# Optimization experiments

Hardware: AMD Instinct MI355X
Metric: run time of the kernel (lower is better)

The kernel has to match this reference:

```python
import jax, jax.numpy as jnp
import numpy as np

B, L, H, D, N, R, K = 1, 2048, 2048, 4096, 16, 128, 4


def setup_inputs() -> dict:
    key = jax.random.key(0)
    ks = jax.random.split(key, 10)
    s = 0.02
    x = jax.random.normal(ks[0], (B, L, H), dtype=jnp.float32)
    W_in = jax.random.normal(ks[1], (H, 2 * D), dtype=jnp.float32) * s
    conv_w = jax.random.normal(ks[2], (K, D), dtype=jnp.float32) * s  # depthwise causal conv
    conv_b = jnp.zeros((D,), dtype=jnp.float32)
    W_x = jax.random.normal(ks[3], (D, R + 2 * N), dtype=jnp.float32) * s
    W_dt = jax.random.normal(ks[4], (R, D), dtype=jnp.float32) * (R ** -0.5)
    # dt bias initialized so softplus(b_dt) ~ dt in [1e-3, 1e-1]
    dt = jnp.exp(jax.random.uniform(ks[5], (D,)) * (np.log(0.1) - np.log(1e-3)) + np.log(1e-3))
    b_dt = dt + jnp.log(-jnp.expm1(-dt))
    A_log = jnp.broadcast_to(jnp.log(jnp.arange(1, N + 1, dtype=jnp.float32)), (D, N))
    D_param = jnp.ones((D,), dtype=jnp.float32)
    W_out = jax.random.normal(ks[6], (D, H), dtype=jnp.float32) * s
    return {"x": x, "W_in": W_in, "conv_w": conv_w, "conv_b": conv_b,
            "W_x": W_x, "W_dt": W_dt, "b_dt": b_dt, "A_log": A_log,
            "D_param": D_param, "W_out": W_out}


def _mamba_fwd(x, W_in, conv_w, conv_b, W_x, W_dt, b_dt, A_log, D_param, W_out):
    silu = jax.nn.silu
    # in_proj then chunk into hidden / gate: [B,L,D] each
    proj = x @ W_in
    hs, gate = jnp.split(proj, 2, axis=-1)
    # causal depthwise conv along sequence (pad K-1 on the left)
    hs_pad = jnp.pad(hs, ((0, 0), (K - 1, 0), (0, 0)))
    conv = sum(hs_pad[:, k:k + L, :] * conv_w[k] for k in range(K)) + conv_b
    hs = silu(conv)  # [B,L,D]
    # ssm parameters
    ssm_p = hs @ W_x  # [B,L,R+2N]
    dt_in, Bm, Cm = jnp.split(ssm_p, [R, R + N], axis=-1)
    dt = jax.nn.softplus(dt_in @ W_dt + b_dt)  # [B,L,D]
    A = -jnp.exp(A_log)  # [D,N]
    dA = jnp.exp(dt[..., None] * A)                       # [B,L,D,N]
    dBu = dt[..., None] * Bm[:, :, None, :] * hs[..., None]  # [B,L,D,N]

    def step(s, inp):
        dA_t, dBu_t, C_t = inp
        s = dA_t * s + dBu_t                 # [B,D,N]
        y = jnp.einsum('bdn,bn->bd', s, C_t)
        return s, y

    s0 = jnp.zeros((B, D, N), dtype=x.dtype)
    xs = (jnp.moveaxis(dA, 1, 0), jnp.moveaxis(dBu, 1, 0), jnp.moveaxis(Cm, 1, 0))
    _, ys = jax.lax.scan(step, s0, xs)       # [L,B,D]
    y = jnp.moveaxis(ys, 0, 1)               # [B,L,D]
    y = y + hs * D_param
    y = y * silu(gate)
    return y @ W_out                          # [B,L,H]


def reference(x, W_in, conv_w, conv_b, W_x, W_dt, b_dt, A_log, D_param, W_out):
    return _mamba_fwd(x, W_in, conv_w, conv_b, W_x, W_dt, b_dt, A_log, D_param, W_out)
```

## Files before the change

### kernel.cpp

```cpp
#include <hip/hip_runtime.h>
#include <hip/hip_bf16.h>

typedef short short8 __attribute__((ext_vector_type(8)));
typedef float floatx4 __attribute__((ext_vector_type(4)));
using bf16 = __hip_bfloat16;

static constexpr int L = 2048, H = 2048, D = 4096, NS = 16, R = 128, KC = 4;
static constexpr int CCH = 64, TCH = L / CCH;
static constexpr int KSP = 16, KCHUNK = 4096 / KSP;
static constexpr int ZOUT = 4, KOUT = 4096 / ZOUT;

__device__ __forceinline__ void g2lds16(const void* g, void* l) {
  __builtin_amdgcn_global_load_lds((const __attribute__((address_space(1))) unsigned int*)g,
                                   (__attribute__((address_space(3))) unsigned int*)l,
                                   16, 0, 0);
}

__global__ void cast_f2b(const float* __restrict__ in, bf16* __restrict__ out, int n) {
  int i = blockIdx.x * 256 + threadIdx.x;
  if (i < n) out[i] = __float2bfloat16(in[i]);
}

__global__ void transpose_cast(const float* __restrict__ in, bf16* __restrict__ out,
                               int Rr, int Cc) {
  __shared__ float tile[32][33];
  int c0 = blockIdx.x * 32, r0 = blockIdx.y * 32;
  int tx = threadIdx.x, ty = threadIdx.y;
#pragma unroll
  for (int i = 0; i < 32; i += 8)
    tile[ty + i][tx] = in[(size_t)(r0 + ty + i) * Cc + (c0 + tx)];
  __syncthreads();
#pragma unroll
  for (int i = 0; i < 32; i += 8)
    out[(size_t)(c0 + ty + i) * Rr + (r0 + tx)] = __float2bfloat16(tile[tx][ty + i]);
}

template <int MODE>
__global__ __launch_bounds__(256) void gemm_async(
    const bf16* __restrict__ A, int lda,
    const bf16* __restrict__ Bt, int ldb,
    bf16* __restrict__ Cb, bf16* __restrict__ Cb2, int ldc, int K) {
  __shared__ short As[2 * 128 * 32];
  __shared__ short Bs[2 * 128 * 32];
  const int m0 = blockIdx.y * 128, n0 = blockIdx.x * 128;
  const int kbeg = (MODE == 3) ? blockIdx.z * K : 0;
  const int tid = threadIdx.x;
  const int lane = tid & 63;
  const int wave = tid >> 6;
  const int wm = (wave >> 1) * 64, wn = (wave & 1) * 64;
  const int lr = lane & 15, kq = lane >> 4;
  const int sr = lane >> 2, sc = (lane & 3) * 8;

  const bf16* Ab = A + (size_t)(m0 + wave * 16 + sr) * lda + sc;
  const bf16* Bb = Bt + (size_t)(n0 + wave * 16 + sr) * ldb + sc;
  short* Asw = &As[wave * 16 * 32];
  short* Bsw = &Bs[wave * 16 * 32];

  floatx4 acc[4][4];
#pragma unroll
  for (int i = 0; i < 4; i++)
#pragma unroll
    for (int j = 0; j < 4; j++)
#pragma unroll
      for (int r = 0; r < 4; r++) acc[i][j][r] = 0.f;

  for (int k0 = kbeg; k0 < kbeg + K; k0 += 64) {
    __syncthreads();
#pragma unroll
    for (int h = 0; h < 2; h++) {
      int kk = k0 + h * 32;
#pragma unroll
      for (int j = 0; j < 2; j++) {
        g2lds16(Ab + (size_t)j * 64 * lda + kk, Asw + h * 4096 + j * 64 * 32);
        g2lds16(Bb + (size_t)j * 64 * ldb + kk, Bsw + h * 4096 + j * 64 * 32);
      }
    }
    __syncthreads();
#pragma unroll
    for (int h = 0; h < 2; h++) {
      short8 af[4], bfr[4];
#pragma unroll
      for (int i = 0; i < 4; i++)
        af[i] = *(const short8*)(&As[h * 4096 + (wm + i * 16 + lr) * 32 + kq * 8]);
#pragma unroll
      for (int j = 0; j < 4; j++)
        bfr[j] = *(const short8*)(&Bs[h * 4096 + (wn + j * 16 + lr) * 32 + kq * 8]);
#pragma unroll
      for (int i = 0; i < 4; i++)
#pragma unroll
        for (int j = 0; j < 4; j++)
          acc[i][j] = __builtin_amdgcn_mfma_f32_16x16x32_bf16(af[i], bfr[j], acc[i][j], 0, 0, 0);
    }
  }

  bf16* base = Cb;
  int coff = 0, ld = ldc;
  if (MODE == 2) {
    if (n0 >= D) { base = Cb2; coff = D; }
    ld = D;
  }
  if (MODE == 3) base = Cb + (size_t)blockIdx.z * L * ldc;
  const int rb = kq * 4;
#pragma unroll
  for (int i = 0; i < 4; i++)
#pragma unroll
    for (int j = 0; j < 4; j++) {
      int col = n0 + wn + j * 16 + lr - coff;
      int row = m0 + wm + i * 16 + rb;
#pragma unroll
      for (int r = 0; r < 4; r++)
        base[(size_t)(row + r) * ld + col] = __float2bfloat16(acc[i][j][r]);
    }
}

__global__ void out_reduce(const unsigned short* __restrict__ P, float* __restrict__ out) {
  int i = blockIdx.x * 256 + threadIdx.x;
  const size_t LH = (size_t)L * H;
  float acc[8];
#pragma unroll
  for (int e = 0; e < 8; e++) acc[e] = 0.f;
#pragma unroll
  for (int z = 0; z < ZOUT; z++) {
    short8 v = *(const short8*)(P + z * LH + (size_t)i * 8);
#pragma unroll
    for (int e = 0; e < 8; e++)
      acc[e] += __uint_as_float(((unsigned)(unsigned short)v[e]) << 16);
  }
#pragma unroll
  for (int q = 0; q < 2; q++) {
    floatx4 o;
#pragma unroll
    for (int r = 0; r < 4; r++) o[r] = acc[q * 4 + r];
    *(floatx4*)(out + (size_t)i * 8 + q * 4) = o;
  }
}

__global__ __launch_bounds__(256) void gemm_splitk(
    const bf16* __restrict__ A, int lda,
    const bf16* __restrict__ Bt, int ldb,
    float* __restrict__ P, int ldc, int N) {
  __shared__ short As[128 * 40];
  __shared__ short Bs[128 * 40];
  const int m0 = blockIdx.y * 128, n0 = blockIdx.x * 128;
  const int kbeg = blockIdx.z * KCHUNK;
  float* C = P + (size_t)blockIdx.z * L * ldc;
  const int tid = threadIdx.x;
  const int lane = tid & 63;
  const int wave = tid >> 6;
  const int wm = (wave >> 1) * 64, wn = (wave & 1) * 64;
  const int lr = lane & 15, kq = lane >> 4;
  const int srow = tid >> 2, scol = (tid & 3) * 8;

  floatx4 acc[4][4];
#pragma unroll
  for (int i = 0; i < 4; i++)
#pragma unroll
    for (int j = 0; j < 4; j++)
#pragma unroll
      for (int r = 0; r < 4; r++) acc[i][j][r] = 0.f;

  for (int k0 = kbeg; k0 < kbeg + KCHUNK; k0 += 32) {
    __syncthreads();
#pragma unroll
    for (int h = 0; h < 2; h++) {
      int r = srow + h * 64;
      short8 va = *(const short8*)((const short*)A + (size_t)(m0 + r) * lda + k0 + scol);
      *(short8*)(&As[r * 40 + scol]) = va;
    }
#pragma unroll
    for (int h = 0; h < 2; h++) {
      int r = srow + h * 64;
      short8 vb;
      if ((n0 + r) < N) {
        vb = *(const short8*)((const short*)Bt + (size_t)(n0 + r) * ldb + k0 + scol);
      } else {
#pragma unroll
        for (int q = 0; q < 8; q++) vb[q] = 0;
      }
      *(short8*)(&Bs[r * 40 + scol]) = vb;
    }
    __syncthreads();
    short8 af[4], bfr[4];
#pragma unroll
    for (int i = 0; i < 4; i++)
      af[i] = *(const short8*)(&As[(wm + i * 16 + lr) * 40 + kq * 8]);
#pragma unroll
    for (int j = 0; j < 4; j++)
      bfr[j] = *(const short8*)(&Bs[(wn + j * 16 + lr) * 40 + kq * 8]);
#pragma unroll
    for (int i = 0; i < 4; i++)
#pragma unroll
      for (int j = 0; j < 4; j++)
        acc[i][j] = __builtin_amdgcn_mfma_f32_16x16x32_bf16(af[i], bfr[j], acc[i][j], 0, 0, 0);
  }

  const int rb = kq * 4;
#pragma unroll
  for (int i = 0; i < 4; i++)
#pragma unroll
    for (int j = 0; j < 4; j++) {
      int col = n0 + wn + j * 16 + lr;
      if (col >= N) continue;
      int row = m0 + wm + i * 16 + rb;
#pragma unroll
      for (int r = 0; r < 4; r++)
        C[(size_t)(row + r) * ldc + col] = acc[i][j][r];
    }
}

__global__ void splitk_reduce(const float* __restrict__ P, float* __restrict__ ssmp,
                              bf16* __restrict__ dtin) {
  int idx = blockIdx.x * 256 + threadIdx.x;
  float s = 0.f;
#pragma unroll
  for (int z = 0; z < KSP; z++) s += P[(size_t)z * L * 160 + idx];
  ssmp[idx] = s;
  int t = idx / 160, c = idx - t * 160;
  if (c < R) dtin[t * R + c] = __float2bfloat16(s);
}

__global__ void conv_silu(const bf16* __restrict__ projh,
                          const float* __restrict__ conv_w, const float* __restrict__ conv_b,
                          bf16* __restrict__ hs_b) {
  int idx = blockIdx.x * 256 + threadIdx.x;
  int d = idx & (D - 1), t = idx >> 12;
  float acc = conv_b[d];
#pragma unroll
  for (int k = 0; k < KC; k++) {
    int tt = t + k - (KC - 1);
    if (tt >= 0) acc += __bfloat162float(projh[(size_t)tt * D + d]) * conv_w[k * D + d];
  }
  float s = acc / (1.f + __expf(-acc));
  hs_b[idx] = __float2bfloat16(s);
}

__device__ __forceinline__ float softplusf(float v) {
  return (v > 20.f) ? v : log1pf(__expf(v));
}

__global__ __launch_bounds__(256) void scan_phase1(
    const bf16* __restrict__ dtraw, const float* __restrict__ b_dt,
    const bf16* __restrict__ hs_b, const float* __restrict__ ssmp,
    const float* __restrict__ A_log,
    float* __restrict__ sdt_out, float* __restrict__ S_out) {
  const int d = blockIdx.x * 256 + threadIdx.x;
  const int c = blockIdx.y;
  float An[NS];
#pragma unroll
  for (int n = 0; n < NS; n++) An[n] = -__expf(A_log[d * NS + n]);
  const float bdt = b_dt[d];
  float s[NS];
#pragma unroll
  for (int n = 0; n < NS; n++) s[n] = 0.f;
  float sdt = 0.f;
  const int t0 = c * TCH;
#pragma unroll 2
  for (int t = t0; t < t0 + TCH; t++) {
    float dtv = softplusf(__bfloat162float(dtraw[(size_t)t * D + d]) + bdt);
    float hsv = __bfloat162float(hs_b[(size_t)t * D + d]);
    sdt += dtv;
    float u = dtv * hsv;
    const float* Bp = ssmp + (size_t)t * 160 + 128;
#pragma unroll
    for (int n = 0; n < NS; n++) {
      float dA = __expf(An[n] * dtv);
      s[n] = dA * s[n] + Bp[n] * u;
    }
  }
  sdt_out[(size_t)c * D + d] = sdt;
  float* Sp = S_out + ((size_t)c * D + d) * NS;
#pragma unroll
  for (int n = 0; n < NS; n += 4)
    *(floatx4*)(Sp + n) = *(floatx4*)(s + n);
}

__global__ __launch_bounds__(256) void scan_phase2(
    const float* __restrict__ sdt, const float* __restrict__ S,
    const float* __restrict__ A_log, float* __restrict__ I) {
  int g = blockIdx.x * 256 + threadIdx.x;
  int d = g >> 4;
  float An = -__expf(A_log[g]);
  float cur = 0.f;
  float sdt_n = sdt[d];
  float S_n = S[g];
  for (int c = 0; c < CCH; c++) {
    float sdt_c = sdt_n, S_c = S_n;
    if (c + 1 < CCH) {
      sdt_n = sdt[(size_t)(c + 1) * D + d];
      S_n = S[(size_t)(c + 1) * D * NS + g];
    }
    I[(size_t)c * D * NS + g] = cur;
    cur = __expf(An * sdt_c) * cur + S_c;
  }
}

__global__ __launch_bounds__(256) void scan_phase3(
    const bf16* __restrict__ dtraw, const float* __restrict__ b_dt,
    const bf16* __restrict__ hs_b, const float* __restrict__ ssmp,
    const bf16* __restrict__ gate_b, const float* __restrict__ A_log,
    const float* __restrict__ D_param, const float* __restrict__ I,
    bf16* __restrict__ y_b) {
  const int d = blockIdx.x * 256 + threadIdx.x;
  const int c = blockIdx.y;
  float An[NS];
#pragma unroll
  for (int n = 0; n < NS; n++) An[n] = -__expf(A_log[d * NS + n]);
  const float bdt = b_dt[d];
  const float Dp = D_param[d];
  float s[NS];
  const float* Ip = I + ((size_t)c * D + d) * NS;
#pragma unroll
  for (int n = 0; n < NS; n += 4)
    *(floatx4*)(s + n) = *(const floatx4*)(Ip + n);
  const int t0 = c * TCH;
#pragma unroll 2
  for (int t = t0; t < t0 + TCH; t++) {
    float dtv = softplusf(__bfloat162float(dtraw[(size_t)t * D + d]) + bdt);
    float hsv = __bfloat162float(hs_b[(size_t)t * D + d]);
    float u = dtv * hsv;
    const float* Bp = ssmp + (size_t)t * 160 + 128;
    const float* Cp = ssmp + (size_t)t * 160 + 144;
    float y = 0.f;
#pragma unroll
    for (int n = 0; n < NS; n++) {
      float dA = __expf(An[n] * dtv);
      s[n] = dA * s[n] + Bp[n] * u;
      y += s[n] * Cp[n];
    }
    float gv = __bfloat162float(gate_b[(size_t)t * D + d]);
    float yv = (y + hsv * Dp) * (gv / (1.f + __expf(-gv)));
    y_b[(size_t)t * D + d] = __float2bfloat16(yv);
  }
}

extern "C" void kernel_launch(void* const* d_in, const int* in_sizes, int n_in,
                              void* d_out, int out_size, void* d_ws, size_t ws_size,
                              hipStream_t stream) {
  const float* x      = (const float*)d_in[0];
  const float* W_in   = (const float*)d_in[1];
  const float* conv_w = (const float*)d_in[2];
  const float* conv_b = (const float*)d_in[3];
  const float* W_x    = (const float*)d_in[4];
  const float* W_dt   = (const float*)d_in[5];
  const float* b_dt   = (const float*)d_in[6];
  const float* A_log  = (const float*)d_in[7];
  const float* D_par  = (const float*)d_in[8];
  const float* W_out  = (const float*)d_in[9];
  float* outp = (float*)d_out;

  char* ws = (char*)d_ws;
  size_t off = 0;
  auto alloc = [&](size_t bytes) {
    char* p = ws + off;
    off += (bytes + 255) & ~(size_t)255;
    return (void*)p;
  };
  bf16*  gate_b  = (bf16*) alloc((size_t)L * D * 2);
  bf16*  hs_b    = (bf16*) alloc((size_t)L * D * 2);
  float* ssmp    = (float*)alloc((size_t)L * 160 * 4);
  bf16*  dtin_b  = (bf16*) alloc((size_t)L * R * 2);
  bf16*  dtbuf_b = (bf16*) alloc((size_t)L * D * 2);
  bf16*  y_b     = (bf16*) alloc((size_t)L * D * 2);
  bf16*  WoutT   = (bf16*) alloc((size_t)H * D * 2);
  float* sdt     = (float*)alloc((size_t)CCH * D * 4);
  float* Sbuf    = (float*)alloc((size_t)CCH * D * NS * 4);
  float* Ibuf    = (float*)alloc((size_t)CCH * D * NS * 4);
  size_t tbase = off;
  bf16*  x_b     = (bf16*) alloc((size_t)L * H * 2);
  bf16*  WinT    = (bf16*) alloc((size_t)2 * D * H * 2);
  bf16*  WxT     = (bf16*) alloc((size_t)160 * D * 2);
  bf16*  WdtT    = (bf16*) alloc((size_t)D * R * 2);
  bf16*  projh_b = (bf16*) alloc((size_t)L * D * 2);
  float* part    = (float*)alloc((size_t)KSP * L * 160 * 4);
  bf16*  part2   = (bf16*)(ws + tbase);

  cast_f2b<<<(L * H) / 256, 256, 0, stream>>>(x, x_b, L * H);

  dim3 tb(32, 8);
  transpose_cast<<<dim3((2 * D) / 32, H / 32), tb, 0, stream>>>(W_in, WinT, H, 2 * D);
  transpose_cast<<<dim3(H / 32, D / 32), tb, 0, stream>>>(W_out, WoutT, D, H);
  transpose_cast<<<dim3(160 / 32, D / 32), tb, 0, stream>>>(W_x, WxT, D, 160);
  transpose_cast<<<dim3(D / 32, R / 32), tb, 0, stream>>>(W_dt, WdtT, R, D);

  gemm_async<2><<<dim3((2 * D) / 128, L / 128), 256, 0, stream>>>(
      x_b, H, WinT, H, projh_b, gate_b, D, H);
  conv_silu<<<(L * D) / 256, 256, 0, stream>>>(projh_b, conv_w, conv_b, hs_b);
  gemm_splitk<<<dim3(2, L / 128, KSP), 256, 0, stream>>>(
      hs_b, D, WxT, D, part, 160, 160);
  splitk_reduce<<<(L * 160) / 256, 256, 0, stream>>>(part, ssmp, dtin_b);
  gemm_async<1><<<dim3(D / 128, L / 128), 256, 0, stream>>>(
      dtin_b, R, WdtT, R, dtbuf_b, nullptr, D, R);

  scan_phase1<<<dim3(D / 256, CCH), 256, 0, stream>>>(
      dtbuf_b, b_dt, hs_b, ssmp, A_log, sdt, Sbuf);
  scan_phase2<<<(D * NS) / 256, 256, 0, stream>>>(sdt, Sbuf, A_log, Ibuf);
  scan_phase3<<<dim3(D / 256, CCH), 256, 0, stream>>>(
      dtbuf_b, b_dt, hs_b, ssmp, gate_b, A_log, D_par, Ibuf, y_b);

  gemm_async<3><<<dim3(H / 128, L / 128, ZOUT), 256, 0, stream>>>(
      y_b, D, WoutT, D, part2, nullptr, H, KOUT);
  out_reduce<<<(L * H) / (256 * 8), 256, 0, stream>>>((const unsigned short*)part2, outp);
}
```

Before: 510.5 us.

## Use 256x256 tile GEMM with 8 waves, LDS swizzle and deeper prefetch for projections

```diff
diff --git a/kernel.cpp b/kernel.cpp
--- a/kernel.cpp
+++ b/kernel.cpp
@@ -33,6 +33,151 @@
 #pragma unroll
   for (int i = 0; i < 32; i += 8)
     out[(size_t)(c0 + ty + i) * Rr + (r0 + tx)] = __float2bfloat16(tile[tx][ty + i]);
+}
+
+template <int MODE>
+__global__ __launch_bounds__(512, 2) void gemm256(
+    const bf16* __restrict__ A, int lda,
+    const bf16* __restrict__ Bt, int ldb,
+    bf16* __restrict__ Cb, bf16* __restrict__ Cb2, int ldc, int K) {
+  __shared__ short As[4 * 8192];
+  __shared__ short Bs[4 * 8192];
+
+  const int gx = gridDim.x;
+  const int nwg = gx * gridDim.y;
+  int id = blockIdx.y * gx + blockIdx.x;
+  id = (id & 7) * (nwg >> 3) + (id >> 3);
+  const int n0 = (id % gx) * 256;
+  const int m0 = (id / gx) * 256;
+  const int kbeg = (MODE == 3) ? blockIdx.z * K : 0;
+  const int NT = K >> 6;
+
+  const int tid = threadIdx.x;
+  const int lane = tid & 63;
+  const int w = tid >> 6;
+  const int wm2 = w >> 2, wn4 = w & 3;
+  const int lr = lane & 15, kq = lane >> 4;
+  const int swzr = ((lane >> 3) & 1) << 1;
+  const int ardo = (wm2 * 128 + lr) * 32 + (kq ^ swzr) * 8;
+  const int brdo = (wn4 * 64 + lr) * 32 + (kq ^ swzr) * 8;
+  const int srow = w * 16 + (lane >> 2);
+  const int swzs = ((lane >> 5) & 1) << 1;
+  const int scol = ((lane & 3) ^ swzs) * 8;
+
+  floatx4 acc[8][4];
+#pragma unroll
+  for (int i = 0; i < 8; i++)
+#pragma unroll
+    for (int j = 0; j < 4; j++)
+#pragma unroll
+      for (int r = 0; r < 4; r++) acc[i][j][r] = 0.f;
+
+  auto stageA = [&](short* pan, int kc) {
+    const bf16* g = A + (size_t)(m0 + srow) * lda + (kbeg + kc + scol);
+    g2lds16(g, pan + w * 512);
+    g2lds16(g + (size_t)128 * lda, pan + 4096 + w * 512);
+  };
+  auto stageB = [&](short* pan, int kc) {
+    const bf16* g = Bt + (size_t)(n0 + srow) * ldb + (kbeg + kc + scol);
+    g2lds16(g, pan + w * 512);
+    g2lds16(g + (size_t)128 * ldb, pan + 4096 + w * 512);
+  };
+
+#define LDA4(pan, base)                                               \
+  _Pragma("unroll") for (int ii = 0; ii < 4; ii++)                    \
+      af[ii] = *(const short8*)((pan) + ardo + ((base) + ii) * 512);
+#define LDB4(pan)                                                     \
+  _Pragma("unroll") for (int jj = 0; jj < 4; jj++)                    \
+      bfr[jj] = *(const short8*)((pan) + brdo + jj * 512);
+#define MFMA4(base)                                                   \
+  _Pragma("unroll") for (int ii = 0; ii < 4; ii++)                    \
+      _Pragma("unroll") for (int jj = 0; jj < 4; jj++)                \
+          acc[(base) + ii][jj] = __builtin_amdgcn_mfma_f32_16x16x32_bf16( \
+              af[ii], bfr[jj], acc[(base) + ii][jj], 0, 0, 0);
+#define PHASE_SYNC()                                                  \
+  __builtin_amdgcn_s_barrier();                                       \
+  asm volatile("s_waitcnt lgkmcnt(0)" ::: "memory");                  \
+  __builtin_amdgcn_sched_barrier(0);
+
+  stageA(As + 0 * 8192, 0);
+  stageB(Bs + 0 * 8192, 0);
+  stageA(As + 1 * 8192, 32);
+  stageB(Bs + 1 * 8192, 32);
+  stageA(As + 2 * 8192, 64);
+  stageB(Bs + 2 * 8192, 64);
+  asm volatile("s_waitcnt vmcnt(4)" ::: "memory");
+  __builtin_amdgcn_s_barrier();
+
+#define GTILE(t, par)                                                      \
+  {                                                                        \
+    short* Ak0 = As + (par) * 16384;                                       \
+    short* Bk0 = Bs + (par) * 16384;                                       \
+    short* Ak1 = Ak0 + 8192;                                               \
+    short* Bk1 = Bk0 + 8192;                                               \
+    short* An1 = As + (1 - (par)) * 16384 + 8192;                          \
+    short* Bn1 = Bs + (1 - (par)) * 16384 + 8192;                          \
+    short8 af[4], bfr[4];                                                  \
+                                           \
+    LDA4(Ak0, 0); LDB4(Bk0);                                               \
+    if ((t) + 1 < NT) stageA(An1, ((t) + 1) * 64 + 32);                    \
+    PHASE_SYNC();                                                          \
+    __builtin_amdgcn_s_setprio(1); MFMA4(0); __builtin_amdgcn_s_setprio(0);\
+    __builtin_amdgcn_s_barrier();                                          \
+                                           \
+    LDA4(Ak0, 4);                                                          \
+    if ((t) + 1 < NT) stageB(Bn1, ((t) + 1) * 64 + 32);                    \
+    PHASE_SYNC();                                                          \
+    __builtin_amdgcn_s_setprio(1); MFMA4(4); __builtin_amdgcn_s_setprio(0);\
+    __builtin_amdgcn_s_barrier();                                          \
+                                           \
+    LDA4(Ak1, 0); LDB4(Bk1);                                               \
+    if ((t) + 2 < NT) stageA(Ak0, ((t) + 2) * 64);                         \
+    PHASE_SYNC();                                                          \
+    __builtin_amdgcn_s_setprio(1); MFMA4(0); __builtin_amdgcn_s_setprio(0);\
+    __builtin_amdgcn_s_barrier();                                          \
+                                           \
+    LDA4(Ak1, 4);                                                          \
+    if ((t) + 2 < NT) stageB(Bk0, ((t) + 2) * 64);                         \
+    PHASE_SYNC();                                                          \
+    __builtin_amdgcn_s_setprio(1); MFMA4(4); __builtin_amdgcn_s_setprio(0);\
+    __builtin_amdgcn_sched_barrier(0);                                     \
+    if ((t) < NT - 2) {                                                    \
+      asm volatile("s_waitcnt vmcnt(4)" ::: "memory");                     \
+    } else {                                                               \
+      asm volatile("s_waitcnt vmcnt(0)" ::: "memory");                     \
+    }                                                                      \
+    __builtin_amdgcn_sched_barrier(0);                                     \
+    __builtin_amdgcn_s_barrier();                                          \
+  }
+
+  for (int t = 0; t < NT; t += 2) {
+    GTILE(t, 0);
+    GTILE(t + 1, 1);
+  }
+#undef GTILE
+#undef PHASE_SYNC
+#undef MFMA4
+#undef LDB4
+#undef LDA4
+
+  bf16* base = Cb;
+  int coff = 0, ld = ldc;
+  if (MODE == 2) {
+    if (n0 >= D) { base = Cb2; coff = D; }
+    ld = D;
+  }
+  if (MODE == 3) base = Cb + (size_t)blockIdx.z * L * ldc;
+  const int rb = kq * 4;
+#pragma unroll
+  for (int i = 0; i < 8; i++)
+#pragma unroll
+    for (int j = 0; j < 4; j++) {
+      int col = n0 + wn4 * 64 + j * 16 + lr - coff;
+      int row = m0 + wm2 * 128 + i * 16 + rb;
+#pragma unroll
+      for (int r = 0; r < 4; r++)
+        base[(size_t)(row + r) * ld + col] = __float2bfloat16(acc[i][j][r]);
+    }
 }
 
 template <int MODE>
@@ -382,7 +527,7 @@
   transpose_cast<<<dim3(160 / 32, D / 32), tb, 0, stream>>>(W_x, WxT, D, 160);
   transpose_cast<<<dim3(D / 32, R / 32), tb, 0, stream>>>(W_dt, WdtT, R, D);
 
-  gemm_async<2><<<dim3((2 * D) / 128, L / 128), 256, 0, stream>>>(
+  gemm256<2><<<dim3((2 * D) / 256, L / 256), 512, 0, stream>>>(
       x_b, H, WinT, H, projh_b, gate_b, D, H);
   conv_silu<<<(L * D) / 256, 256, 0, stream>>>(projh_b, conv_w, conv_b, hs_b);
   gemm_splitk<<<dim3(2, L / 128, KSP), 256, 0, stream>>>(
@@ -397,7 +542,7 @@
   scan_phase3<<<dim3(D / 256, CCH), 256, 0, stream>>>(
       dtbuf_b, b_dt, hs_b, ssmp, gate_b, A_log, D_par, Ibuf, y_b);
 
-  gemm_async<3><<<dim3(H / 128, L / 128, ZOUT), 256, 0, stream>>>(
+  gemm256<3><<<dim3(H / 256, L / 256, ZOUT), 512, 0, stream>>>(
       y_b, D, WoutT, D, part2, nullptr, H, KOUT);
   out_reduce<<<(L * H) / (256 * 8), 256, 0, stream>>>((const unsigned short*)part2, outp);
 }
```

New measurement: 476.3 us. -6.7%, faster.
